# Kernel tuning notes

Hardware: AMD Instinct MI355X
Metric: run time of the kernel (lower is better)

The kernel has to match this reference:

```python
import jax, jax.numpy as jnp
import numpy as np

EMBED, HEADS, LEVELS, POINTS = 256, 8, 4, 4
SPATIAL_SHAPES = np.array([[128, 128], [64, 64], [32, 32], [16, 16]], dtype=np.int32)


def _grid_init_bias():
    # Faithful reproduction of the sampling_offsets bias init (per-head directional grid).
    thetas = np.arange(HEADS, dtype=np.float32) * (2.0 * np.pi / HEADS)
    g = np.stack([np.cos(thetas), np.sin(thetas)], -1)
    g = g / np.abs(g).max(-1, keepdims=True)
    g = np.tile(g.reshape(HEADS, 1, 1, 2), (1, LEVELS, POINTS, 1))
    for i in range(POINTS):
        g[:, :, i, :] *= i + 1
    return g.reshape(-1).astype(np.float32)


def setup_inputs() -> dict:
    key = jax.random.key(0)
    ks = jax.random.split(key, 8)
    bs = 2
    V = int((SPATIAL_SHAPES[:, 0] * SPATIAL_SHAPES[:, 1]).sum())  # 21760
    Q = V  # encoder self-attention
    C = EMBED
    n_off = HEADS * LEVELS * POINTS * 2
    n_attn = HEADS * LEVELS * POINTS
    inv_sqrt_c = 1.0 / np.sqrt(C)
    return {
        "query": jax.random.normal(ks[0], (bs, Q, C), jnp.float32),
        "value": jax.random.normal(ks[1], (bs, V, C), jnp.float32),
        "reference_points": jax.random.uniform(ks[2], (bs, Q, LEVELS, 2), jnp.float32),
        "spatial_shapes": SPATIAL_SHAPES,  # static int array
        # learned parameters (torch Linear stored as [in, out]: y = x @ W + b)
        "W_off": jax.random.normal(ks[3], (C, n_off), jnp.float32) * 0.01,
        "b_off": jnp.asarray(_grid_init_bias()),
        "W_attn": jax.random.normal(ks[4], (C, n_attn), jnp.float32) * 0.02,
        "b_attn": jnp.zeros((n_attn,), jnp.float32),
        "W_v": jax.random.normal(ks[5], (C, C), jnp.float32) * inv_sqrt_c,
        "b_v": jnp.zeros((C,), jnp.float32),
        "W_out": jax.random.normal(ks[6], (C, C), jnp.float32) * inv_sqrt_c,
        "b_out": jnp.zeros((C,), jnp.float32),
    }


def _ms_deform_attn(query, value, reference_points, shapes,
                    W_off, b_off, W_attn, b_attn, W_v, b_v, W_out, b_out):
    bs, Q, C = query.shape
    d = C // HEADS
    # value projection -> [bs, heads, V, d]
    val = (value @ W_v + b_v).reshape(bs, -1, HEADS, d).transpose(0, 2, 1, 3)
    # sampling offsets and attention weights from query
    off = (query @ W_off + b_off).reshape(bs, Q, HEADS, LEVELS, POINTS, 2)
    attn = jax.nn.softmax(
        (query @ W_attn + b_attn).reshape(bs, Q, HEADS, LEVELS * POINTS), axis=-1
    ).reshape(bs, Q, HEADS, LEVELS, POINTS)
    # offset normalizer is (W, H) per level
    norm = jnp.asarray(np.stack([shapes[:, 1], shapes[:, 0]], -1), jnp.float32)  # [L,2]
    loc = reference_points[:, :, None, :, None, :] + off / norm[None, None, None, :, None, :]

    out = jnp.zeros((bs, HEADS, Q, d), query.dtype)
    start = 0
    for l in range(LEVELS):
        H, W = int(shapes[l, 0]), int(shapes[l, 1])
        v_l = val[:, :, start:start + H * W]  # [bs, heads, H*W, d]
        start += H * W
        loc_l = loc[:, :, :, l]    # [bs, Q, heads, P, 2] in [0,1]
        attn_l = attn[:, :, :, l]  # [bs, Q, heads, P]
        # grid_sample(align_corners=False, padding_mode='zeros') semantics
        g = 2.0 * loc_l - 1.0
        x = (g[..., 0] + 1.0) * 0.5 * W - 0.5
        y = (g[..., 1] + 1.0) * 0.5 * H - 0.5
        x0 = jnp.floor(x)
        y0 = jnp.floor(y)
        for dx in (0, 1):
            for dy in (0, 1):
                xi = x0 + dx
                yi = y0 + dy
                w = (1.0 - jnp.abs(x - xi)) * (1.0 - jnp.abs(y - yi))
                valid = (xi >= 0) & (xi <= W - 1) & (yi >= 0) & (yi <= H - 1)
                w = jnp.where(valid, w, 0.0) * attn_l  # fused corner + attention weight
                idx = (jnp.clip(yi, 0, H - 1).astype(jnp.int32) * W
                       + jnp.clip(xi, 0, W - 1).astype(jnp.int32))  # [bs,Q,heads,P]
                idx_t = jnp.transpose(idx, (0, 2, 1, 3)).reshape(bs, HEADS, Q * POINTS)
                vals = jnp.take_along_axis(v_l, idx_t[..., None], axis=2)
                vals = vals.reshape(bs, HEADS, Q, POINTS, d)
                out = out + jnp.einsum('bhqpd,bqhp->bhqd', vals, w)
    out = out.transpose(0, 2, 1, 3).reshape(bs, Q, C)  # heads-major channel layout
    return out @ W_out + b_out


def reference(query, value, reference_points, spatial_shapes,
              W_off, b_off, W_attn, b_attn, W_v, b_v, W_out, b_out):
    shapes = np.asarray(spatial_shapes)  # static
    return _ms_deform_attn(query, value, reference_points, shapes,
                           W_off, b_off, W_attn, b_attn, W_v, b_v, W_out, b_out)
```

## Files before the change

### kernel.cpp

```cpp
#include <hip/hip_runtime.h>
#include <math.h>

#define QN 21760
#define MTOT 43520
#define SZBQC 11141120

typedef __attribute__((ext_vector_type(8))) short bf16x8;
typedef __attribute__((ext_vector_type(4))) float f32x4;

__device__ inline ushort f2bf(float f) {
  union { float f; uint u; } v; v.f = f;
  return (ushort)((v.u + 0x7FFFu + ((v.u >> 16) & 1u)) >> 16);
}
__device__ inline uint pk2(float lo, float hi) { return (uint)f2bf(lo) | ((uint)f2bf(hi) << 16); }

__device__ inline void g2l(const ushort* g, ushort* l) {
  __builtin_amdgcn_global_load_lds(
      (const __attribute__((address_space(1))) void*)g,
      (__attribute__((address_space(3))) void*)l, 16, 0, 0);
}

__global__ __launch_bounds__(256) void prep_weights(
    const float* __restrict__ Wv, const float* __restrict__ Wout,
    const float* __restrict__ Woff, const float* __restrict__ Wattn,
    const float* __restrict__ boff, const float* __restrict__ battn,
    ushort* __restrict__ wv_t, ushort* __restrict__ wout_t,
    ushort* __restrict__ wol_t, float* __restrict__ biasf) {
  int bidx = blockIdx.x, t = threadIdx.x;
  if (bidx < 256) {
    int idx = bidx * 256 + t; int n = idx >> 8, k = idx & 255;
    wv_t[idx] = f2bf(Wv[(size_t)k * 256 + n]);
  } else if (bidx < 512) {
    int idx = (bidx - 256) * 256 + t; int n = idx >> 8, k = idx & 255;
    wout_t[idx] = f2bf(Wout[(size_t)k * 256 + n]);
  } else {
    int idx = (bidx - 512) * 256 + t; int n = idx >> 8, k = idx & 255;
    float v = (n < 256) ? Woff[(size_t)k * 256 + n] : Wattn[(size_t)k * 128 + (n - 256)];
    wol_t[idx] = f2bf(v);
    if (idx < 384) biasf[idx] = (idx < 256) ? boff[idx] : battn[idx - 256];
  }
}


__global__ __launch_bounds__(256) void gemm_in(
    const float* __restrict__ value, const float* __restrict__ query,
    const ushort* __restrict__ Wv, const ushort* __restrict__ Wol,
    const float* __restrict__ bv, const float* __restrict__ bol,
    ushort* __restrict__ val_out, float* __restrict__ offlog) {
  __shared__ ushort As[2][4096];
  __shared__ ushort Bs[2][4096];
  const int t = threadIdx.x, wave = t >> 6, lane = t & 63;
  const int bx = blockIdx.y, bm = blockIdx.x * 128;
  const bool isVal = bx < 2;
  const float* A   = isVal ? value : query;
  const ushort* Bt = isVal ? (Wv + (size_t)bx * 128 * 256)
                           : (Wol + (size_t)(bx - 2) * 128 * 256);
  const int wm = (wave >> 1) * 64, wn = (wave & 1) * 64;
  const int l15 = lane & 15, l4 = lane >> 4;
  const int pc = l4 ^ ((l15 >> 1) & 3);

  const int srow = lane >> 2;
  const int sch  = (lane & 3) ^ ((lane >> 3) & 3);
  const ushort* Bg = Bt + (size_t)(32 * wave + srow) * 256 + sch * 8;
  ushort* lb[2] = { &Bs[0][(32 * wave) * 32], &Bs[1][(32 * wave) * 32] };

  f32x4 acc[4][4];
#pragma unroll
  for (int i = 0; i < 4; ++i)
#pragma unroll
    for (int j = 0; j < 4; ++j) acc[i][j] = (f32x4){0.f, 0.f, 0.f, 0.f};

  int arow[4], apart[4];
#pragma unroll
  for (int i = 0; i < 4; ++i) {
    int c = t + i * 256; arow[i] = c >> 3; apart[i] = c & 7;
  }

  {
    float4 pa[4];
#pragma unroll
    for (int i = 0; i < 4; ++i)
      pa[i] = *(const float4*)&A[(size_t)(bm + arow[i]) * 256 + apart[i] * 4];
    g2l(Bg, lb[0]); g2l(Bg + 16 * 256, lb[0] + 16 * 32);
#pragma unroll
    for (int i = 0; i < 4; ++i) {
      int pc16 = (apart[i] >> 1) ^ ((arow[i] >> 1) & 3);
      ushort4 hv = { f2bf(pa[i].x), f2bf(pa[i].y), f2bf(pa[i].z), f2bf(pa[i].w) };
      *(ushort4*)&As[0][arow[i] * 32 + pc16 * 8 + (apart[i] & 1) * 4] = hv;
    }
  }

  for (int k = 0; k < 8; ++k) {
    __syncthreads();
    const int cur = k & 1, nxt = cur ^ 1;
    float4 pa[4];
    if (k < 7) {
      int k1 = (k + 1) * 32;
#pragma unroll
      for (int i = 0; i < 4; ++i)
        pa[i] = *(const float4*)&A[(size_t)(bm + arow[i]) * 256 + k1 + apart[i] * 4];
      g2l(Bg + k1, lb[nxt]); g2l(Bg + 16 * 256 + k1, lb[nxt] + 16 * 32);
    }
    bf16x8 af[4], bfr[4];
#pragma unroll
    for (int mi = 0; mi < 4; ++mi)
      af[mi] = *(const bf16x8*)&As[cur][(wm + mi * 16 + l15) * 32 + pc * 8];
#pragma unroll
    for (int ni = 0; ni < 4; ++ni)
      bfr[ni] = *(const bf16x8*)&Bs[cur][(wn + ni * 16 + l15) * 32 + pc * 8];
#pragma unroll
    for (int mi = 0; mi < 4; ++mi)
#pragma unroll
      for (int ni = 0; ni < 4; ++ni)
        acc[mi][ni] = __builtin_amdgcn_mfma_f32_16x16x32_bf16(af[mi], bfr[ni], acc[mi][ni], 0, 0, 0);
    if (k < 7) {
#pragma unroll
      for (int i = 0; i < 4; ++i) {
        int pc16 = (apart[i] >> 1) ^ ((arow[i] >> 1) & 3);
        ushort4 hv = { f2bf(pa[i].x), f2bf(pa[i].y), f2bf(pa[i].z), f2bf(pa[i].w) };
        *(ushort4*)&As[nxt][arow[i] * 32 + pc16 * 8 + (apart[i] & 1) * 4] = hv;
      }
    }
  }

  if (isVal) {
    _Float16* vo = (_Float16*)val_out;
#pragma unroll
    for (int mi = 0; mi < 4; ++mi)
#pragma unroll
      for (int ni = 0; ni < 4; ++ni) {
        int col = bx * 128 + wn + ni * 16 + l15;
        float bb = bv[col];
        int hh = col >> 5, c = col & 31;
#pragma unroll
        for (int r = 0; r < 4; ++r) {
          int row = bm + wm + mi * 16 + l4 * 4 + r;
          int b = (row >= QN) ? 1 : 0;
          int vpos = row - b * QN;
          vo[((size_t)(b * 8 + hh) * QN + vpos) * 32 + c] = (_Float16)(acc[mi][ni][r] + bb);
        }
      }
  } else {
#pragma unroll
    for (int mi = 0; mi < 4; ++mi)
#pragma unroll
      for (int ni = 0; ni < 4; ++ni) {
        int col = (bx - 2) * 128 + wn + ni * 16 + l15;
        float bb = bol[col];
#pragma unroll
        for (int r = 0; r < 4; ++r) {
          int row = bm + wm + mi * 16 + l4 * 4 + r;
          offlog[(size_t)row * 384 + col] = acc[mi][ni][r] + bb;
        }
      }
  }
}

__global__ __launch_bounds__(256) void gemm_out(
    const ushort* __restrict__ A, const ushort* __restrict__ Bt,
    const float* __restrict__ bias, float* __restrict__ C) {
  __shared__ ushort As[2][4096];
  __shared__ ushort Bs[2][4096];
  const int t = threadIdx.x, wave = t >> 6, lane = t & 63;
  const int bm = blockIdx.x * 128, bn = blockIdx.y * 128;
  const int wm = (wave >> 1) * 64, wn = (wave & 1) * 64;
  const int l15 = lane & 15, l4 = lane >> 4;
  const int pc = l4 ^ ((l15 >> 1) & 3);

  const int srow = lane >> 2;
  const int sch  = (lane & 3) ^ ((lane >> 3) & 3);
  const ushort* Ag = A + (size_t)(bm + 32 * wave + srow) * 256 + sch * 8;
  const ushort* Bg = Bt + (size_t)(bn + 32 * wave + srow) * 256 + sch * 8;
  ushort* la[2] = { &As[0][(32 * wave) * 32], &As[1][(32 * wave) * 32] };
  ushort* lb[2] = { &Bs[0][(32 * wave) * 32], &Bs[1][(32 * wave) * 32] };

  f32x4 acc[4][4];
#pragma unroll
  for (int i = 0; i < 4; ++i)
#pragma unroll
    for (int j = 0; j < 4; ++j) acc[i][j] = (f32x4){0.f, 0.f, 0.f, 0.f};

  g2l(Ag, la[0]); g2l(Ag + 16 * 256, la[0] + 16 * 32);
  g2l(Bg, lb[0]); g2l(Bg + 16 * 256, lb[0] + 16 * 32);

  for (int k = 0; k < 8; ++k) {
    __syncthreads();
    const int cur = k & 1, nxt = cur ^ 1;
    if (k < 7) {
      int k1 = (k + 1) * 32;
      g2l(Ag + k1, la[nxt]); g2l(Ag + 16 * 256 + k1, la[nxt] + 16 * 32);
      g2l(Bg + k1, lb[nxt]); g2l(Bg + 16 * 256 + k1, lb[nxt] + 16 * 32);
    }
    bf16x8 af[4], bfr[4];
#pragma unroll
    for (int mi = 0; mi < 4; ++mi)
      af[mi] = *(const bf16x8*)&As[cur][(wm + mi * 16 + l15) * 32 + pc * 8];
#pragma unroll
    for (int ni = 0; ni < 4; ++ni)
      bfr[ni] = *(const bf16x8*)&Bs[cur][(wn + ni * 16 + l15) * 32 + pc * 8];
#pragma unroll
    for (int mi = 0; mi < 4; ++mi)
#pragma unroll
      for (int ni = 0; ni < 4; ++ni)
        acc[mi][ni] = __builtin_amdgcn_mfma_f32_16x16x32_bf16(af[mi], bfr[ni], acc[mi][ni], 0, 0, 0);
  }

#pragma unroll
  for (int mi = 0; mi < 4; ++mi)
#pragma unroll
    for (int ni = 0; ni < 4; ++ni) {
      int col = bn + wn + ni * 16 + l15;
      float bb = bias[col];
#pragma unroll
      for (int r = 0; r < 4; ++r) {
        int row = bm + wm + mi * 16 + l4 * 4 + r;
        C[(size_t)row * 256 + col] = acc[mi][ni][r] + bb;
      }
    }
}

__device__ inline void fmah(float* a, uint4 u, float wv) {
  union { uint4 u; _Float16 h[8]; } c; c.u = u;
#pragma unroll
  for (int i = 0; i < 8; ++i) a[i] = fmaf((float)c.h[i], wv, a[i]);
}

__global__ __launch_bounds__(256) void msda_sample(
    const ushort* __restrict__ val, const float* __restrict__ offlog,
    const float* __restrict__ ref, ushort* __restrict__ interm) {
  int h   = blockIdx.x & 7;
  int z   = blockIdx.x >> 3;
  int s   = threadIdx.x & 7;
  int o   = s & 3;
  int pp  = s >> 2;
  bool xs = s >= 4;
  int bq  = z * 32 + (threadIdx.x >> 3);
  int b   = (bq >= QN) ? 1 : 0;
  const ushort* vbl = val + (size_t)((uint)(b * 8 + h) * (uint)QN) * 32u + (uint)(s * 8);

  const float* lgp = offlog + (size_t)bq * 384 + 256 + h * 16;
  float2 lg = *(const float2*)(lgp + o * 4 + pp * 2);
  float m = fmaxf(lg.x, lg.y);
  m = fmaxf(m, __shfl_xor(m, 1, 64));
  m = fmaxf(m, __shfl_xor(m, 2, 64));
  m = fmaxf(m, __shfl_xor(m, 4, 64));
  float e0 = __expf(lg.x - m), e1 = __expf(lg.y - m);
  float ssum = e0 + e1;
  ssum += __shfl_xor(ssum, 1, 64);
  ssum += __shfl_xor(ssum, 2, 64);
  ssum += __shfl_xor(ssum, 4, 64);
  float inv = __builtin_amdgcn_rcpf(ssum);
  float aw0 = e0 * inv, aw1 = e1 * inv;

  const int  Wl  = 128 >> o;
  const uint t16 = 65536u >> (o + o);
  const int  lst = (int)((65536u - t16) / 3u);
  const float fW = (float)Wl;
  const float* offp = offlog + (size_t)bq * 384 + h * 32;
  float4 f0 = *(const float4*)(offp + o * 8 + pp * 4);
  float2 rf = *(const float2*)(ref + (size_t)bq * 8 + o * 2);
  const float xb = rf.x * fW - 0.5f;
  const float yb = rf.y * fW - 0.5f;
  float ox[2] = { f0.x, f0.z };
  float oy[2] = { f0.y, f0.w };
  float awq[2] = { aw0, aw1 };

  uint  pA0[2], pA1[2];
  float pW0[2], pW1[2], pY0[2], pY1[2];
#pragma unroll
  for (int q = 0; q < 2; ++q) {
    float x = xb + ox[q], y = yb + oy[q];
    float x0f = floorf(x), y0f = floorf(y);
    float fx = x - x0f, fy = y - y0f;
    int x0 = (int)x0f, y0 = (int)y0f;
    float a = awq[q];
    float wx0 = ((uint)x0       < (uint)Wl) ? (1.f - fx) : 0.f;
    float wx1 = ((uint)(x0 + 1) < (uint)Wl) ? fx         : 0.f;
    pY0[q] = (((uint)y0       < (uint)Wl) ? (1.f - fy) : 0.f) * a;
    pY1[q] = (((uint)(y0 + 1) < (uint)Wl) ? fy         : 0.f) * a;
    int xc0 = min(max(x0, 0), Wl - 1);
    int xc1 = min(max(x0 + 1, 0), Wl - 1);
    int yc0 = min(max(y0, 0), Wl - 1);
    int yc1 = min(max(y0 + 1, 0), Wl - 1);
    int xbase = min(max(x0, 0), Wl - 2);
    pW0[q] = ((xbase     == xc0) ? wx0 : 0.f) + ((xbase     == xc1) ? wx1 : 0.f);
    pW1[q] = ((xbase + 1 == xc0) ? wx0 : 0.f) + ((xbase + 1 == xc1) ? wx1 : 0.f);
    pA0[q] = (uint)((lst + yc0 * Wl + xbase) * 32);
    pA1[q] = (uint)((lst + yc1 * Wl + xbase) * 32);
  }

  float acc[8];
#pragma unroll
  for (int i = 0; i < 8; ++i) acc[i] = 0.f;

  const int gb = (threadIdx.x & 63) & ~7;

  uint  bA0[2], bA1[2];
  float bW[2], bY0[2], bY1[2];
  uint4 u0[2], u1[2];

#define MSDA_BCAST(J, S) do {                                   \
    const int l_ = (J) >> 2, p_ = (J) & 3;                      \
    const int src_ = gb | ((p_ >> 1) << 2) | l_;                \
    const int q_ = p_ & 1;                                      \
    bA0[S] = (uint)__shfl((int)pA0[q_], src_, 64);              \
    bA1[S] = (uint)__shfl((int)pA1[q_], src_, 64);              \
    float w0_ = __shfl(pW0[q_], src_, 64);                      \
    float w1_ = __shfl(pW1[q_], src_, 64);                      \
    bW[S]  = xs ? w1_ : w0_;                                    \
    bY0[S] = __shfl(pY0[q_], src_, 64);                         \
    bY1[S] = __shfl(pY1[q_], src_, 64);                         \
  } while (0)
#define MSDA_LOAD(S) do {                                       \
    u0[S] = *(const uint4*)(vbl + bA0[S]);                      \
    u1[S] = *(const uint4*)(vbl + bA1[S]);                      \
  } while (0)

  MSDA_BCAST(0, 0);
  MSDA_LOAD(0);
#pragma unroll
  for (int j = 0; j < 16; ++j) {
    const int cur = j & 1, nxt = cur ^ 1;
    if (j < 15) { MSDA_BCAST(j + 1, nxt); MSDA_LOAD(nxt); }
    fmah(acc, u0[cur], bW[cur] * bY0[cur]);
    fmah(acc, u1[cur], bW[cur] * bY1[cur]);
  }
#undef MSDA_BCAST
#undef MSDA_LOAD

#pragma unroll
  for (int i = 0; i < 8; ++i) acc[i] += __shfl_xor(acc[i], 4, 64);

  uint2 ov;
  if (!xs) { ov.x = pk2(acc[0], acc[1]); ov.y = pk2(acc[2], acc[3]); }
  else     { ov.x = pk2(acc[4], acc[5]); ov.y = pk2(acc[6], acc[7]); }
  *(uint2*)(interm + (size_t)bq * 256 + h * 32 + (s & 3) * 8 + (xs ? 4 : 0)) = ov;
}

extern "C" void kernel_launch(void* const* d_in, const int* in_sizes, int n_in,
                              void* d_out, int out_size, void* d_ws, size_t ws_size,
                              hipStream_t stream) {
  const float* query = (const float*)d_in[0];
  const float* value = (const float*)d_in[1];
  const float* ref   = (const float*)d_in[2];
  const float* W_off  = (const float*)d_in[4];
  const float* b_off  = (const float*)d_in[5];
  const float* W_attn = (const float*)d_in[6];
  const float* b_attn = (const float*)d_in[7];
  const float* W_v    = (const float*)d_in[8];
  const float* b_v    = (const float*)d_in[9];
  const float* W_out  = (const float*)d_in[10];
  const float* b_out  = (const float*)d_in[11];
  float* out = (float*)d_out;

  char* wsb = (char*)d_ws;
  ushort* ws_wv     = (ushort*)(wsb + 0);
  ushort* ws_wol    = (ushort*)(wsb + 131072);
  ushort* ws_wout   = (ushort*)(wsb + 327680);
  float*  ws_biasf  = (float*)(wsb + 458752);
  ushort* ws_val    = (ushort*)(wsb + 462848);
  ushort* ws_interm = (ushort*)(wsb + 22745088);
  float*  ws_offlog = (float*)(wsb + 45027328);
  size_t need = (size_t)45027328 + 66846720;
  if (ws_size < need) return;

  dim3 blk(256);
  prep_weights<<<dim3(896), blk, 0, stream>>>(W_v, W_out, W_off, W_attn, b_off, b_attn,
                                              ws_wv, ws_wout, ws_wol, ws_biasf);
  gemm_in<<<dim3(340, 5), blk, 0, stream>>>(value, query, ws_wv, ws_wol, b_v, ws_biasf,
                                            ws_val, ws_offlog);
  msda_sample<<<dim3(10880), blk, 0, stream>>>(ws_val, ws_offlog, ref, ws_interm);
  gemm_out<<<dim3(340, 2), blk, 0, stream>>>(ws_interm, ws_wout, b_out, out);
}
```

Before: 266.5 us.

## Fuse all four stages into one cooperative persistent kernel with grid syncs

New measurement: 262.2 us. No clear change (-1.6%).

```diff
diff --git a/kernel.cpp b/kernel.cpp
--- a/kernel.cpp
+++ b/kernel.cpp
@@ -1,5 +1,8 @@
 #include <hip/hip_runtime.h>
+#include <hip/hip_cooperative_groups.h>
 #include <math.h>
+
+namespace cg = cooperative_groups;
 
 #define QN 21760
 #define MTOT 43520
@@ -20,13 +23,14 @@
       (__attribute__((address_space(3))) void*)l, 16, 0, 0);
 }
 
-__global__ __launch_bounds__(256) void prep_weights(
+
+__device__ __forceinline__ void prep_body(
+    int bidx, int t,
     const float* __restrict__ Wv, const float* __restrict__ Wout,
     const float* __restrict__ Woff, const float* __restrict__ Wattn,
     const float* __restrict__ boff, const float* __restrict__ battn,
     ushort* __restrict__ wv_t, ushort* __restrict__ wout_t,
     ushort* __restrict__ wol_t, float* __restrict__ biasf) {
-  int bidx = blockIdx.x, t = threadIdx.x;
   if (bidx < 256) {
     int idx = bidx * 256 + t; int n = idx >> 8, k = idx & 255;
     wv_t[idx] = f2bf(Wv[(size_t)k * 256 + n]);
@@ -42,15 +46,14 @@
 }
 
 
-__global__ __launch_bounds__(256) void gemm_in(
+__device__ __forceinline__ void gemm_in_body(
+    ushort (*As)[4096], ushort (*Bs)[4096], int bxv, int bx, int t,
     const float* __restrict__ value, const float* __restrict__ query,
     const ushort* __restrict__ Wv, const ushort* __restrict__ Wol,
     const float* __restrict__ bv, const float* __restrict__ bol,
     ushort* __restrict__ val_out, float* __restrict__ offlog) {
-  __shared__ ushort As[2][4096];
-  __shared__ ushort Bs[2][4096];
-  const int t = threadIdx.x, wave = t >> 6, lane = t & 63;
-  const int bx = blockIdx.y, bm = blockIdx.x * 128;
+  const int wave = t >> 6, lane = t & 63;
+  const int bm = bxv * 128;
   const bool isVal = bx < 2;
   const float* A   = isVal ? value : query;
   const ushort* Bt = isVal ? (Wv + (size_t)bx * 128 * 256)
@@ -156,13 +159,12 @@
   }
 }
 
-__global__ __launch_bounds__(256) void gemm_out(
+__device__ __forceinline__ void gemm_out_body(
+    ushort (*As)[4096], ushort (*Bs)[4096], int bxv, int byv, int t,
     const ushort* __restrict__ A, const ushort* __restrict__ Bt,
     const float* __restrict__ bias, float* __restrict__ C) {
-  __shared__ ushort As[2][4096];
-  __shared__ ushort Bs[2][4096];
-  const int t = threadIdx.x, wave = t >> 6, lane = t & 63;
-  const int bm = blockIdx.x * 128, bn = blockIdx.y * 128;
+  const int wave = t >> 6, lane = t & 63;
+  const int bm = bxv * 128, bn = byv * 128;
   const int wm = (wave >> 1) * 64, wn = (wave & 1) * 64;
   const int l15 = lane & 15, l4 = lane >> 4;
   const int pc = l4 ^ ((l15 >> 1) & 3);
@@ -219,22 +221,23 @@
     }
 }
 
-__device__ inline void fmah(float* a, uint4 u, float wv) {
+__device__ __forceinline__ void fmah(float* a, uint4 u, float wv) {
   union { uint4 u; _Float16 h[8]; } c; c.u = u;
 #pragma unroll
   for (int i = 0; i < 8; ++i) a[i] = fmaf((float)c.h[i], wv, a[i]);
 }
 
-__global__ __launch_bounds__(256) void msda_sample(
+__device__ __forceinline__ void msda_body(
+    int vb, int tix,
     const ushort* __restrict__ val, const float* __restrict__ offlog,
     const float* __restrict__ ref, ushort* __restrict__ interm) {
-  int h   = blockIdx.x & 7;
-  int z   = blockIdx.x >> 3;
-  int s   = threadIdx.x & 7;
+  int h   = vb & 7;
+  int z   = vb >> 3;
+  int s   = tix & 7;
   int o   = s & 3;
   int pp  = s >> 2;
   bool xs = s >= 4;
-  int bq  = z * 32 + (threadIdx.x >> 3);
+  int bq  = z * 32 + (tix >> 3);
   int b   = (bq >= QN) ? 1 : 0;
   const ushort* vbl = val + (size_t)((uint)(b * 8 + h) * (uint)QN) * 32u + (uint)(s * 8);
 
@@ -293,7 +296,7 @@
 #pragma unroll
   for (int i = 0; i < 8; ++i) acc[i] = 0.f;
 
-  const int gb = (threadIdx.x & 63) & ~7;
+  const int gb = (tix & 63) & ~7;
 
   uint  bA0[2], bA1[2];
   float bW[2], bY0[2], bY1[2];
@@ -337,6 +340,85 @@
   *(uint2*)(interm + (size_t)bq * 256 + h * 32 + (s & 3) * 8 + (xs ? 4 : 0)) = ov;
 }
 
+
+__global__ __launch_bounds__(256) void prep_weights(
+    const float* Wv, const float* Wout, const float* Woff, const float* Wattn,
+    const float* boff, const float* battn,
+    ushort* wv_t, ushort* wout_t, ushort* wol_t, float* biasf) {
+  prep_body(blockIdx.x, threadIdx.x, Wv, Wout, Woff, Wattn, boff, battn,
+            wv_t, wout_t, wol_t, biasf);
+}
+
+__global__ __launch_bounds__(256) void gemm_in(
+    const float* value, const float* query, const ushort* Wv, const ushort* Wol,
+    const float* bv, const float* bol, ushort* val_out, float* offlog) {
+  __shared__ ushort As[2][4096];
+  __shared__ ushort Bs[2][4096];
+  gemm_in_body(As, Bs, blockIdx.x, blockIdx.y, threadIdx.x,
+               value, query, Wv, Wol, bv, bol, val_out, offlog);
+}
+
+__global__ __launch_bounds__(256) void gemm_out(
+    const ushort* A, const ushort* Bt, const float* bias, float* C) {
+  __shared__ ushort As[2][4096];
+  __shared__ ushort Bs[2][4096];
+  gemm_out_body(As, Bs, blockIdx.x, blockIdx.y, threadIdx.x, A, Bt, bias, C);
+}
+
+__global__ __launch_bounds__(256) void msda_sample(
+    const ushort* val, const float* offlog, const float* ref, ushort* interm) {
+  msda_body(blockIdx.x, threadIdx.x, val, offlog, ref, interm);
+}
+
+
+struct FusedArgs {
+  const float *query, *value, *ref;
+  const float *Woff, *boff, *Wattn, *battn, *Wv, *bv, *Wout, *bout;
+  ushort *ws_wv, *ws_wol, *ws_wout;
+  float *ws_biasf;
+  ushort *ws_val, *ws_interm;
+  float *ws_offlog;
+  float *out;
+};
+
+__global__ __launch_bounds__(256) void fused_all(FusedArgs a) {
+  __shared__ ushort As[2][4096];
+  __shared__ ushort Bs[2][4096];
+  cg::grid_group grid = cg::this_grid();
+  const int t = threadIdx.x;
+  const int g0 = blockIdx.x, gs = gridDim.x;
+
+  for (int vb = g0; vb < 896; vb += gs)
+    prep_body(vb, t, a.Wv, a.Wout, a.Woff, a.Wattn, a.boff, a.battn,
+              a.ws_wv, a.ws_wout, a.ws_wol, a.ws_biasf);
+  __builtin_amdgcn_fence(__ATOMIC_RELEASE, "agent");
+  grid.sync();
+  __builtin_amdgcn_fence(__ATOMIC_ACQUIRE, "agent");
+
+  for (int vb = g0; vb < 1700; vb += gs) {
+    gemm_in_body(As, Bs, vb % 340, vb / 340, t,
+                 a.value, a.query, a.ws_wv, a.ws_wol, a.bv, a.ws_biasf,
+                 a.ws_val, a.ws_offlog);
+    __syncthreads();
+  }
+  __builtin_amdgcn_fence(__ATOMIC_RELEASE, "agent");
+  grid.sync();
+  __builtin_amdgcn_fence(__ATOMIC_ACQUIRE, "agent");
+
+  for (int vb = g0; vb < 10880; vb += gs)
+    msda_body(vb, t, a.ws_val, a.ws_offlog, a.ref, a.ws_interm);
+  __builtin_amdgcn_fence(__ATOMIC_RELEASE, "agent");
+  grid.sync();
+  __builtin_amdgcn_fence(__ATOMIC_ACQUIRE, "agent");
+
+  for (int vb = g0; vb < 680; vb += gs) {
+    gemm_out_body(As, Bs, vb % 340, vb / 340, t,
+                  a.ws_interm, a.ws_wout, a.bout, a.out);
+    __syncthreads();
+  }
+}
+
+
 extern "C" void kernel_launch(void* const* d_in, const int* in_sizes, int n_in,
                               void* d_out, int out_size, void* d_ws, size_t ws_size,
                               hipStream_t stream) {
@@ -365,10 +447,32 @@
   if (ws_size < need) return;
 
   dim3 blk(256);
-  prep_weights<<<dim3(896), blk, 0, stream>>>(W_v, W_out, W_off, W_attn, b_off, b_attn,
-                                              ws_wv, ws_wout, ws_wol, ws_biasf);
-  gemm_in<<<dim3(340, 5), blk, 0, stream>>>(value, query, ws_wv, ws_wol, b_v, ws_biasf,
-                                            ws_val, ws_offlog);
-  msda_sample<<<dim3(10880), blk, 0, stream>>>(ws_val, ws_offlog, ref, ws_interm);
-  gemm_out<<<dim3(340, 2), blk, 0, stream>>>(ws_interm, ws_wout, b_out, out);
-}
+
+  bool coop_done = false;
+  int nb = 0;
+  if (hipOccupancyMaxActiveBlocksPerMultiprocessor(&nb, (const void*)fused_all, 256, 0)
+          == hipSuccess && nb > 0) {
+    int grid = nb * 256;
+    if (grid > 4096) grid = 4096;
+    FusedArgs fa;
+    fa.query = query; fa.value = value; fa.ref = ref;
+    fa.Woff = W_off; fa.boff = b_off; fa.Wattn = W_attn; fa.battn = b_attn;
+    fa.Wv = W_v; fa.bv = b_v; fa.Wout = W_out; fa.bout = b_out;
+    fa.ws_wv = ws_wv; fa.ws_wol = ws_wol; fa.ws_wout = ws_wout;
+    fa.ws_biasf = ws_biasf; fa.ws_val = ws_val; fa.ws_interm = ws_interm;
+    fa.ws_offlog = ws_offlog; fa.out = out;
+    void* kargs[] = { (void*)&fa };
+    if (hipLaunchCooperativeKernel((const void*)fused_all, dim3(grid), blk,
+                                   kargs, 0, stream) == hipSuccess)
+      coop_done = true;
+  }
+
+  if (!coop_done) {
+    prep_weights<<<dim3(896), blk, 0, stream>>>(W_v, W_out, W_off, W_attn, b_off, b_attn,
+                                                ws_wv, ws_wout, ws_wol, ws_biasf);
+    gemm_in<<<dim3(340, 5), blk, 0, stream>>>(value, query, ws_wv, ws_wol, b_v, ws_biasf,
+                                              ws_val, ws_offlog);
+    msda_sample<<<dim3(10880), blk, 0, stream>>>(ws_val, ws_offlog, ref, ws_interm);
+    gemm_out<<<dim3(340, 2), blk, 0, stream>>>(ws_interm, ws_wout, b_out, out);
+  }
+}
```

## Cache full bf16 A tile in LDS across N panels; triple-buffer gemm_out

Applied to the files above, without the earlier changes.

Result: no change. 269.5 us (+1.1%).

```diff
diff --git a/kernel.cpp b/kernel.cpp
--- a/kernel.cpp
+++ b/kernel.cpp
@@ -47,28 +47,21 @@
     const ushort* __restrict__ Wv, const ushort* __restrict__ Wol,
     const float* __restrict__ bv, const float* __restrict__ bol,
     ushort* __restrict__ val_out, float* __restrict__ offlog) {
-  __shared__ ushort As[2][4096];
+  __shared__ ushort AsF[8][4096];
   __shared__ ushort Bs[2][4096];
   const int t = threadIdx.x, wave = t >> 6, lane = t & 63;
-  const int bx = blockIdx.y, bm = blockIdx.x * 128;
-  const bool isVal = bx < 2;
-  const float* A   = isVal ? value : query;
-  const ushort* Bt = isVal ? (Wv + (size_t)bx * 128 * 256)
-                           : (Wol + (size_t)(bx - 2) * 128 * 256);
+  const int grp = blockIdx.y;
+  const int bm = blockIdx.x * 128;
+  const float* A = grp ? query : value;
+  const int npan = grp ? 3 : 2;
   const int wm = (wave >> 1) * 64, wn = (wave & 1) * 64;
   const int l15 = lane & 15, l4 = lane >> 4;
   const int pc = l4 ^ ((l15 >> 1) & 3);
 
   const int srow = lane >> 2;
   const int sch  = (lane & 3) ^ ((lane >> 3) & 3);
-  const ushort* Bg = Bt + (size_t)(32 * wave + srow) * 256 + sch * 8;
+  const ushort* Bgbase = (grp ? Wol : Wv) + (size_t)(32 * wave + srow) * 256 + sch * 8;
   ushort* lb[2] = { &Bs[0][(32 * wave) * 32], &Bs[1][(32 * wave) * 32] };
-
-  f32x4 acc[4][4];
-#pragma unroll
-  for (int i = 0; i < 4; ++i)
-#pragma unroll
-    for (int j = 0; j < 4; ++j) acc[i][j] = (f32x4){0.f, 0.f, 0.f, 0.f};
 
   int arow[4], apart[4];
 #pragma unroll
@@ -76,91 +69,96 @@
     int c = t + i * 256; arow[i] = c >> 3; apart[i] = c & 7;
   }
 
-  {
+  g2l(Bgbase, lb[0]); g2l(Bgbase + 16 * 256, lb[0] + 16 * 32);
+
+#pragma unroll
+  for (int k = 0; k < 8; ++k) {
     float4 pa[4];
 #pragma unroll
     for (int i = 0; i < 4; ++i)
-      pa[i] = *(const float4*)&A[(size_t)(bm + arow[i]) * 256 + apart[i] * 4];
-    g2l(Bg, lb[0]); g2l(Bg + 16 * 256, lb[0] + 16 * 32);
+      pa[i] = *(const float4*)&A[(size_t)(bm + arow[i]) * 256 + k * 32 + apart[i] * 4];
 #pragma unroll
     for (int i = 0; i < 4; ++i) {
       int pc16 = (apart[i] >> 1) ^ ((arow[i] >> 1) & 3);
       ushort4 hv = { f2bf(pa[i].x), f2bf(pa[i].y), f2bf(pa[i].z), f2bf(pa[i].w) };
-      *(ushort4*)&As[0][arow[i] * 32 + pc16 * 8 + (apart[i] & 1) * 4] = hv;
-    }
-  }
-
-  for (int k = 0; k < 8; ++k) {
-    __syncthreads();
-    const int cur = k & 1, nxt = cur ^ 1;
-    float4 pa[4];
-    if (k < 7) {
-      int k1 = (k + 1) * 32;
-#pragma unroll
-      for (int i = 0; i < 4; ++i)
-        pa[i] = *(const float4*)&A[(size_t)(bm + arow[i]) * 256 + k1 + apart[i] * 4];
-      g2l(Bg + k1, lb[nxt]); g2l(Bg + 16 * 256 + k1, lb[nxt] + 16 * 32);
-    }
-    bf16x8 af[4], bfr[4];
-#pragma unroll
-    for (int mi = 0; mi < 4; ++mi)
-      af[mi] = *(const bf16x8*)&As[cur][(wm + mi * 16 + l15) * 32 + pc * 8];
-#pragma unroll
-    for (int ni = 0; ni < 4; ++ni)
-      bfr[ni] = *(const bf16x8*)&Bs[cur][(wn + ni * 16 + l15) * 32 + pc * 8];
-#pragma unroll
-    for (int mi = 0; mi < 4; ++mi)
+      *(ushort4*)&AsF[k][arow[i] * 32 + pc16 * 8 + (apart[i] & 1) * 4] = hv;
+    }
+  }
+
+  for (int p = 0; p < npan; ++p) {
+    const ushort* Bg = Bgbase + (size_t)p * 32768;
+    if (p > 0) {
+      g2l(Bg, lb[0]); g2l(Bg + 16 * 256, lb[0] + 16 * 32);
+    }
+
+    f32x4 acc[4][4];
+#pragma unroll
+    for (int i = 0; i < 4; ++i)
+#pragma unroll
+      for (int j = 0; j < 4; ++j) acc[i][j] = (f32x4){0.f, 0.f, 0.f, 0.f};
+
+#pragma unroll
+    for (int k = 0; k < 8; ++k) {
+      __syncthreads();
+      const int cur = k & 1, nxt = cur ^ 1;
+      if (k < 7) {
+        int k1 = (k + 1) * 32;
+        g2l(Bg + k1, lb[nxt]); g2l(Bg + 16 * 256 + k1, lb[nxt] + 16 * 32);
+      }
+      bf16x8 af[4], bfr[4];
+#pragma unroll
+      for (int mi = 0; mi < 4; ++mi)
+        af[mi] = *(const bf16x8*)&AsF[k][(wm + mi * 16 + l15) * 32 + pc * 8];
 #pragma unroll
       for (int ni = 0; ni < 4; ++ni)
-        acc[mi][ni] = __builtin_amdgcn_mfma_f32_16x16x32_bf16(af[mi], bfr[ni], acc[mi][ni], 0, 0, 0);
-    if (k < 7) {
-#pragma unroll
-      for (int i = 0; i < 4; ++i) {
-        int pc16 = (apart[i] >> 1) ^ ((arow[i] >> 1) & 3);
-        ushort4 hv = { f2bf(pa[i].x), f2bf(pa[i].y), f2bf(pa[i].z), f2bf(pa[i].w) };
-        *(ushort4*)&As[nxt][arow[i] * 32 + pc16 * 8 + (apart[i] & 1) * 4] = hv;
-      }
-    }
-  }
-
-  if (isVal) {
-    _Float16* vo = (_Float16*)val_out;
-#pragma unroll
-    for (int mi = 0; mi < 4; ++mi)
-#pragma unroll
-      for (int ni = 0; ni < 4; ++ni) {
-        int col = bx * 128 + wn + ni * 16 + l15;
-        float bb = bv[col];
-        int hh = col >> 5, c = col & 31;
-#pragma unroll
-        for (int r = 0; r < 4; ++r) {
-          int row = bm + wm + mi * 16 + l4 * 4 + r;
-          int b = (row >= QN) ? 1 : 0;
-          int vpos = row - b * QN;
-          vo[((size_t)(b * 8 + hh) * QN + vpos) * 32 + c] = (_Float16)(acc[mi][ni][r] + bb);
+        bfr[ni] = *(const bf16x8*)&Bs[cur][(wn + ni * 16 + l15) * 32 + pc * 8];
+#pragma unroll
+      for (int mi = 0; mi < 4; ++mi)
+#pragma unroll
+        for (int ni = 0; ni < 4; ++ni)
+          acc[mi][ni] = __builtin_amdgcn_mfma_f32_16x16x32_bf16(af[mi], bfr[ni], acc[mi][ni], 0, 0, 0);
+    }
+
+    const int bx = grp ? (2 + p) : p;
+    if (bx < 2) {
+      _Float16* vo = (_Float16*)val_out;
+#pragma unroll
+      for (int mi = 0; mi < 4; ++mi)
+#pragma unroll
+        for (int ni = 0; ni < 4; ++ni) {
+          int col = bx * 128 + wn + ni * 16 + l15;
+          float bb = bv[col];
+          int hh = col >> 5, c = col & 31;
+#pragma unroll
+          for (int r = 0; r < 4; ++r) {
+            int row = bm + wm + mi * 16 + l4 * 4 + r;
+            int b = (row >= QN) ? 1 : 0;
+            int vpos = row - b * QN;
+            vo[((size_t)(b * 8 + hh) * QN + vpos) * 32 + c] = (_Float16)(acc[mi][ni][r] + bb);
+          }
         }
-      }
-  } else {
-#pragma unroll
-    for (int mi = 0; mi < 4; ++mi)
-#pragma unroll
-      for (int ni = 0; ni < 4; ++ni) {
-        int col = (bx - 2) * 128 + wn + ni * 16 + l15;
-        float bb = bol[col];
-#pragma unroll
-        for (int r = 0; r < 4; ++r) {
-          int row = bm + wm + mi * 16 + l4 * 4 + r;
-          offlog[(size_t)row * 384 + col] = acc[mi][ni][r] + bb;
+    } else {
+#pragma unroll
+      for (int mi = 0; mi < 4; ++mi)
+#pragma unroll
+        for (int ni = 0; ni < 4; ++ni) {
+          int col = (bx - 2) * 128 + wn + ni * 16 + l15;
+          float bb = bol[col];
+#pragma unroll
+          for (int r = 0; r < 4; ++r) {
+            int row = bm + wm + mi * 16 + l4 * 4 + r;
+            offlog[(size_t)row * 384 + col] = acc[mi][ni][r] + bb;
+          }
         }
-      }
+    }
   }
 }
 
 __global__ __launch_bounds__(256) void gemm_out(
     const ushort* __restrict__ A, const ushort* __restrict__ Bt,
     const float* __restrict__ bias, float* __restrict__ C) {
-  __shared__ ushort As[2][4096];
-  __shared__ ushort Bs[2][4096];
+  __shared__ ushort As[3][4096];
+  __shared__ ushort Bs[3][4096];
   const int t = threadIdx.x, wave = t >> 6, lane = t & 63;
   const int bm = blockIdx.x * 128, bn = blockIdx.y * 128;
   const int wm = (wave >> 1) * 64, wn = (wave & 1) * 64;
@@ -171,8 +169,10 @@
   const int sch  = (lane & 3) ^ ((lane >> 3) & 3);
   const ushort* Ag = A + (size_t)(bm + 32 * wave + srow) * 256 + sch * 8;
   const ushort* Bg = Bt + (size_t)(bn + 32 * wave + srow) * 256 + sch * 8;
-  ushort* la[2] = { &As[0][(32 * wave) * 32], &As[1][(32 * wave) * 32] };
-  ushort* lb[2] = { &Bs[0][(32 * wave) * 32], &Bs[1][(32 * wave) * 32] };
+  ushort* la[3] = { &As[0][(32 * wave) * 32], &As[1][(32 * wave) * 32],
+                    &As[2][(32 * wave) * 32] };
+  ushort* lb[3] = { &Bs[0][(32 * wave) * 32], &Bs[1][(32 * wave) * 32],
+                    &Bs[2][(32 * wave) * 32] };
 
   f32x4 acc[4][4];
 #pragma unroll
@@ -180,24 +180,32 @@
 #pragma unroll
     for (int j = 0; j < 4; ++j) acc[i][j] = (f32x4){0.f, 0.f, 0.f, 0.f};
 
-  g2l(Ag, la[0]); g2l(Ag + 16 * 256, la[0] + 16 * 32);
-  g2l(Bg, lb[0]); g2l(Bg + 16 * 256, lb[0] + 16 * 32);
-
+  g2l(Ag, la[0]);      g2l(Ag + 16 * 256, la[0] + 16 * 32);
+  g2l(Bg, lb[0]);      g2l(Bg + 16 * 256, lb[0] + 16 * 32);
+  g2l(Ag + 32, la[1]); g2l(Ag + 16 * 256 + 32, la[1] + 16 * 32);
+  g2l(Bg + 32, lb[1]); g2l(Bg + 16 * 256 + 32, lb[1] + 16 * 32);
+
+#pragma unroll
   for (int k = 0; k < 8; ++k) {
-    __syncthreads();
-    const int cur = k & 1, nxt = cur ^ 1;
-    if (k < 7) {
-      int k1 = (k + 1) * 32;
-      g2l(Ag + k1, la[nxt]); g2l(Ag + 16 * 256 + k1, la[nxt] + 16 * 32);
-      g2l(Bg + k1, lb[nxt]); g2l(Bg + 16 * 256 + k1, lb[nxt] + 16 * 32);
+    const int cb = k % 3;
+    const int sb = (k + 2) % 3;
+    if (k < 7) { asm volatile("s_waitcnt vmcnt(4)" ::: "memory"); }
+    else       { asm volatile("s_waitcnt vmcnt(0)" ::: "memory"); }
+    __builtin_amdgcn_sched_barrier(0);
+    __builtin_amdgcn_s_barrier();
+    __builtin_amdgcn_sched_barrier(0);
+    if (k + 2 <= 7) {
+      int k2 = (k + 2) * 32;
+      g2l(Ag + k2, la[sb]); g2l(Ag + 16 * 256 + k2, la[sb] + 16 * 32);
+      g2l(Bg + k2, lb[sb]); g2l(Bg + 16 * 256 + k2, lb[sb] + 16 * 32);
     }
     bf16x8 af[4], bfr[4];
 #pragma unroll
     for (int mi = 0; mi < 4; ++mi)
-      af[mi] = *(const bf16x8*)&As[cur][(wm + mi * 16 + l15) * 32 + pc * 8];
+      af[mi] = *(const bf16x8*)&As[cb][(wm + mi * 16 + l15) * 32 + pc * 8];
 #pragma unroll
     for (int ni = 0; ni < 4; ++ni)
-      bfr[ni] = *(const bf16x8*)&Bs[cur][(wn + ni * 16 + l15) * 32 + pc * 8];
+      bfr[ni] = *(const bf16x8*)&Bs[cb][(wn + ni * 16 + l15) * 32 + pc * 8];
 #pragma unroll
     for (int mi = 0; mi < 4; ++mi)
 #pragma unroll
@@ -228,8 +236,9 @@
 __global__ __launch_bounds__(256) void msda_sample(
     const ushort* __restrict__ val, const float* __restrict__ offlog,
     const float* __restrict__ ref, ushort* __restrict__ interm) {
-  int h   = blockIdx.x & 7;
-  int z   = blockIdx.x >> 3;
+  int vb  = blockIdx.x;
+  int h   = vb & 7;
+  int z   = vb >> 3;
   int s   = threadIdx.x & 7;
   int o   = s & 3;
   int pp  = s >> 2;
@@ -367,7 +376,7 @@
   dim3 blk(256);
   prep_weights<<<dim3(896), blk, 0, stream>>>(W_v, W_out, W_off, W_attn, b_off, b_attn,
                                               ws_wv, ws_wout, ws_wol, ws_biasf);
-  gemm_in<<<dim3(340, 5), blk, 0, stream>>>(value, query, ws_wv, ws_wol, b_v, ws_biasf,
+  gemm_in<<<dim3(340, 2), blk, 0, stream>>>(value, query, ws_wv, ws_wol, b_v, ws_biasf,
                                             ws_val, ws_offlog);
   msda_sample<<<dim3(10880), blk, 0, stream>>>(ws_val, ws_offlog, ref, ws_interm);
   gemm_out<<<dim3(340, 2), blk, 0, stream>>>(ws_interm, ws_wout, b_out, out);
```
